# Performance work log

Measured on AMD Instinct MI355X. Metric: run time of the kernel, lower is better.

Reference implementation:

```python
import jax, jax.numpy as jnp
import numpy as np

BS, N, C = 512, 18, 2048
EPS = 1e-12
BN_SCALE = 1.0 / np.sqrt(1.0 + 1e-5)  # eval-mode BN with running_mean=0, running_var=1


def _normalize(v):
    # F.normalize(p=2, dim=2, eps=1e-12)
    n = jnp.linalg.norm(v, axis=2, keepdims=True)
    return v / jnp.maximum(n, EPS)


def _bn_relu(v, gamma, beta):
    # BatchNorm2d in eval mode (running_mean=0, running_var=1) followed by ReLU
    return jax.nn.relu(v * (gamma * BN_SCALE) + beta)


def _safe_sqrt(r):
    # forward-identical to sqrt (r >= 0 here); avoids NaN grad at r == 0 (diagonal)
    pos = r > 0
    return jnp.where(pos, jnp.sqrt(jnp.where(pos, r, 1.0)), 0.0)


def setup_inputs() -> dict:
    key = jax.random.key(0)
    ks = jax.random.split(key, 10)
    s = 0.02
    return {
        "x": jax.random.normal(ks[0], (BS, N, C), jnp.float32),
        "part_coordinate": jax.random.uniform(ks[1], (BS, N, 4), jnp.float32),
        # conv1: C -> 3 (1x1)
        "w1": jax.random.normal(ks[2], (3, C), jnp.float32) * s,
        "b1": jnp.zeros((3,), jnp.float32),
        # conv2: 4 -> C, BN, ReLU, C -> 3
        "w2a": jax.random.normal(ks[3], (C, 4), jnp.float32) * s,
        "b2a": jnp.zeros((C,), jnp.float32),
        "g2": jnp.ones((C,), jnp.float32),
        "be2": jnp.zeros((C,), jnp.float32),
        "w2b": jax.random.normal(ks[4], (3, C), jnp.float32) * s,
        "b2b": jnp.zeros((3,), jnp.float32),
        # conv: C -> C, BN, ReLU
        "wc": jax.random.normal(ks[5], (C, C), jnp.float32) * s,
        "bc": jnp.zeros((C,), jnp.float32),
        "gc": jnp.ones((C,), jnp.float32),
        "bec": jnp.zeros((C,), jnp.float32),
        # conv3: C -> C, BN, ReLU
        "w3": jax.random.normal(ks[6], (C, C), jnp.float32) * s,
        "b3": jnp.zeros((C,), jnp.float32),
        "g3": jnp.ones((C,), jnp.float32),
        "be3": jnp.zeros((C,), jnp.float32),
    }


def reference(x, part_coordinate, w1, b1, w2a, b2a, g2, be2, w2b, b2b,
              wc, bc, gc, bec, w3, b3, g3, be3):
    # z1 = softmax(conv1(x)) over the 3 clusters
    z1 = jax.nn.softmax(jnp.einsum('bnc,kc->bnk', x, w1) + b1, axis=2)  # [B,N,3]

    # distance_list1: cosine affinities of x and z1
    xn = _normalize(x)
    d1_1 = jnp.einsum('bnc,bmc->bnm', xn, xn)       # [B,N,N]
    z1n = _normalize(z1)
    d2_1 = jnp.einsum('bnk,bmk->bnm', z1n, z1n)     # [B,N,N]

    # z2 = softmax(conv2(part_coordinate))
    h = _bn_relu(jnp.einsum('bnf,cf->bnc', part_coordinate, w2a) + b2a, g2, be2)
    z2 = jax.nn.softmax(jnp.einsum('bnc,kc->bnk', h, w2b) + b2b, axis=2)  # [B,N,3]

    # distance_list2: spatial-center distance + cosine affinity of z2
    yc = part_coordinate[..., 0] + jnp.floor(part_coordinate[..., 2] / 2)
    xc = part_coordinate[..., 1] + jnp.floor(part_coordinate[..., 3] / 2)
    dy = (yc[:, None, :] - yc[:, :, None]) ** 2
    dx = (xc[:, None, :] - xc[:, :, None]) ** 2
    d1_2 = 1.0 - 2.0 * _safe_sqrt(dx + dy)          # [B,N,N]
    z2n = _normalize(z2)
    d2_2 = jnp.einsum('bnk,bmk->bnm', z2n, z2n)     # [B,N,N]

    # encode / decode aggregation over 3 cluster nodes
    z = z1 + z2                                      # [B,N,3]
    enc = z / (jnp.sum(z, axis=1, keepdims=True) + EPS)
    dec = z / (jnp.sum(z, axis=2, keepdims=True) + EPS)
    u = jnp.einsum('bnk,bnc->bkc', enc, x)           # [B,3,C]
    u = _bn_relu(jnp.einsum('bkc,dc->bkd', u, wc) + bc, gc, bec)
    y = jnp.einsum('bnk,bkc->bnc', dec, u)           # [B,N,C]
    y = _bn_relu(jnp.einsum('bnc,dc->bnd', y, w3) + b3, g3, be3) + x

    return (y, d2_1, d1_1, d2_2, d1_2)
```

## Files before the change

kernel.cpp:

```cpp
#include <hip/hip_runtime.h>

#define BS   512
#define NPTS 18
#define CH   2048
#define EPSF 1e-12f
#define BNS  0.9999950000374997f

typedef unsigned short ushort_t;
typedef __attribute__((ext_vector_type(8)))  short bfrag;
typedef __attribute__((ext_vector_type(4)))  float f32x4v;
typedef __attribute__((ext_vector_type(16))) float f32x16;

__device__ inline ushort_t bf16_rne(float f) {
  union { float f; unsigned int u; } c; c.f = f;
  unsigned int u = c.u;
  u += 0x7fffu + ((u >> 16) & 1u);
  return (ushort_t)(u >> 16);
}
__device__ inline float bf16_to_f(ushort_t s) {
  union { float f; unsigned int u; } c; c.u = ((unsigned int)s) << 16;
  return c.f;
}
__device__ inline bfrag cvt8(float4 a, float4 b) {
  bfrag r;
  r[0]=(short)bf16_rne(a.x); r[1]=(short)bf16_rne(a.y);
  r[2]=(short)bf16_rne(a.z); r[3]=(short)bf16_rne(a.w);
  r[4]=(short)bf16_rne(b.x); r[5]=(short)bf16_rne(b.y);
  r[6]=(short)bf16_rne(b.z); r[7]=(short)bf16_rne(b.w);
  return r;
}

__global__ __launch_bounds__(256) void k_fused(
    const float* __restrict__ x, const float* __restrict__ pc,
    const float* __restrict__ w1,
    const float* __restrict__ w2a, const float* __restrict__ b2a,
    const float* __restrict__ g2, const float* __restrict__ be2,
    const float* __restrict__ w2b,
    const float* __restrict__ wc, const float* __restrict__ w3,
    ushort_t* __restrict__ wc_bf, ushort_t* __restrict__ w3_bf,
    float* __restrict__ Glp, float* __restrict__ l2p)
{
  const int blk = blockIdx.x, tid = threadIdx.x;

  if (blk >= BS*4) {
    const int cb = blk - BS*4;
    const int n4 = CH*CH/4;
    #pragma unroll
    for (int k = 0; k < 4; k++) {
      int gid = (cb*4 + k)*256 + tid;
      const float* src; ushort_t* dst; int i;
      if (gid < n4) { src = wc; dst = wc_bf; i = gid; }
      else          { src = w3; dst = w3_bf; i = gid - n4; }
      float4 v = ((const float4*)src)[i];
      ushort4 o;
      o.x = bf16_rne(v.x); o.y = bf16_rne(v.y);
      o.z = bf16_rne(v.z); o.w = bf16_rne(v.w);
      ((ushort4*)dst)[i] = o;
    }
    return;
  }

  __shared__ float Gt[4][378];
  const int bq = blk, b = bq >> 2, q = bq & 3;
  const int lane = tid & 63, wv = tid >> 6;

  {
    const int rc = lane & 31, kh = lane >> 5;
    const int arow = (rc < NPTS) ? rc : (NPTS-1);
    const bool isw = (rc >= NPTS) && (rc < NPTS+3);
    const int wrow = isw ? (rc - NPTS) : 0;
    const float* xp = x + ((size_t)b*NPTS + arow)*CH + q*512 + wv*128 + kh*8;
    const float* wp = w1 + (size_t)wrow*CH + q*512 + wv*128 + kh*8;
    f32x16 acc0 = {0.f,0.f,0.f,0.f,0.f,0.f,0.f,0.f,0.f,0.f,0.f,0.f,0.f,0.f,0.f,0.f};
    f32x16 acc1 = acc0;
    #pragma unroll
    for (int j = 0; j < 8; j++) {
      const int kb = j*16;
      bfrag av = cvt8(*(const float4*)(xp + kb), *(const float4*)(xp + kb + 4));
      bfrag bv = av;
      if (isw) bv = cvt8(*(const float4*)(wp + kb), *(const float4*)(wp + kb + 4));
      if (j & 1) acc1 = __builtin_amdgcn_mfma_f32_32x32x16_bf16(av, bv, acc1, 0, 0, 0);
      else       acc0 = __builtin_amdgcn_mfma_f32_32x32x16_bf16(av, bv, acc0, 0, 0, 0);
    }
    #pragma unroll
    for (int r = 0; r < 16; r++) {
      int orow = (r & 3) + 8*(r >> 2) + 4*kh;
      if (orow < NPTS && rc < 21) Gt[wv][orow*21 + rc] = acc0[r] + acc1[r];
    }
  }

  {
    const int p0 = wv*5;
    const int np = (wv == 3) ? 3 : 5;
    float4 pq[5];
    #pragma unroll
    for (int j = 0; j < 5; j++)
      pq[j] = *(const float4*)(pc + (size_t)b*NPTS*4 + (p0 + (j < np ? j : 0))*4);
    float acc[5][3];
    #pragma unroll
    for (int j = 0; j < 5; j++) { acc[j][0]=0.f; acc[j][1]=0.f; acc[j][2]=0.f; }
    #pragma unroll 2
    for (int it = 0; it < 8; it++) {
      int c = q*512 + it*64 + lane;
      const float4 wa = *(const float4*)(w2a + (size_t)c*4);
      float bb = b2a[c], gg = g2[c]*BNS, be = be2[c];
      float wb0 = w2b[c], wb1 = w2b[CH+c], wb2 = w2b[2*CH+c];
      #pragma unroll
      for (int j = 0; j < 5; j++) {
        float v = fmaf(pq[j].w, wa.w, fmaf(pq[j].z, wa.z,
                  fmaf(pq[j].y, wa.y, fmaf(pq[j].x, wa.x, bb))));
        float h = fmaxf(fmaf(v, gg, be), 0.f);
        acc[j][0] = fmaf(h, wb0, acc[j][0]);
        acc[j][1] = fmaf(h, wb1, acc[j][1]);
        acc[j][2] = fmaf(h, wb2, acc[j][2]);
      }
    }
    #pragma unroll
    for (int j = 0; j < 5; j++) {
      if (j < np) {
        #pragma unroll
        for (int k = 0; k < 3; k++) {
          float v = acc[j][k];
          #pragma unroll
          for (int off = 32; off; off >>= 1) v += __shfl_xor(v, off);
          if (lane == 0) l2p[(size_t)bq*54 + (p0+j)*3 + k] = v;
        }
      }
    }
  }

  __syncthreads();
  for (int t = tid; t < 378; t += 256) {
    float* g = Glp + (size_t)bq*378;
    g[t] = (Gt[0][t] + Gt[1][t]) + (Gt[2][t] + Gt[3][t]);
  }
}

__global__ __launch_bounds__(512) void k_final(
    const float* __restrict__ x, const float* __restrict__ pc,
    const float* __restrict__ b1, const float* __restrict__ b2b,
    const float* __restrict__ Glp, const float* __restrict__ l2p,
    float* __restrict__ d21, float* __restrict__ d11,
    float* __restrict__ d22, float* __restrict__ d12,
    ushort_t* __restrict__ u_pre, float* __restrict__ dec_out)
{
  __shared__ float sGl[378];
  __shared__ float l2s[54];
  __shared__ float z1s[54], z2s[54], encs[54];
  __shared__ float ycs[NPTS], xcs[NPTS];
  __shared__ float n1inv[NPTS], n2inv[NPTS], rinv[NPTS], colinv[3];
  const int b = blockIdx.x, tid = threadIdx.x;

  if (tid < 378) {
    const float* g = Glp + (size_t)b*4*378 + tid;
    sGl[tid] = (g[0] + g[378]) + (g[756] + g[1134]);
  } else if (tid < 432) {
    int t = tid - 378;
    const float* g = l2p + (size_t)b*4*54 + t;
    l2s[t] = (g[0] + g[54]) + (g[108] + g[162]) + b2b[t%3];
  } else if (tid < 450) {
    int n = tid - 432;
    const float* p = pc + (size_t)b*NPTS*4 + n*4;
    ycs[n] = p[0] + floorf(p[2]*0.5f);
    xcs[n] = p[1] + floorf(p[3]*0.5f);
  }
  __syncthreads();

  if (tid < NPTS) {
    int n = tid;
    float a0 = sGl[n*21+18] + b1[0], a1 = sGl[n*21+19] + b1[1], a2 = sGl[n*21+20] + b1[2];
    float mx = fmaxf(a0, fmaxf(a1, a2));
    float e0 = expf(a0-mx), e1 = expf(a1-mx), e2 = expf(a2-mx);
    float inv = 1.f/(e0+e1+e2);
    float z10 = e0*inv, z11 = e1*inv, z12 = e2*inv;
    z1s[n*3+0]=z10; z1s[n*3+1]=z11; z1s[n*3+2]=z12;
    n1inv[n] = 1.f/fmaxf(sqrtf(z10*z10+z11*z11+z12*z12), EPSF);

    float c0 = l2s[n*3+0], c1 = l2s[n*3+1], c2 = l2s[n*3+2];
    mx = fmaxf(c0, fmaxf(c1, c2));
    e0 = expf(c0-mx); e1 = expf(c1-mx); e2 = expf(c2-mx);
    inv = 1.f/(e0+e1+e2);
    float z20 = e0*inv, z21 = e1*inv, z22 = e2*inv;
    z2s[n*3+0]=z20; z2s[n*3+1]=z21; z2s[n*3+2]=z22;
    n2inv[n] = 1.f/fmaxf(sqrtf(z20*z20+z21*z21+z22*z22), EPSF);

    float zr0 = z10+z20, zr1 = z11+z21, zr2 = z12+z22;
    float rinvv = 1.f/((zr0+zr1+zr2) + EPSF);
    dec_out[(size_t)b*54 + n*3 + 0] = zr0*rinvv;
    dec_out[(size_t)b*54 + n*3 + 1] = zr1*rinvv;
    dec_out[(size_t)b*54 + n*3 + 2] = zr2*rinvv;

    rinv[n] = 1.f/fmaxf(sqrtf(sGl[n*21+n]), EPSF);
  }
  __syncthreads();

  if (tid < 3) {
    float s = 0.f;
    #pragma unroll
    for (int n = 0; n < NPTS; n++) s += z1s[n*3+tid] + z2s[n*3+tid];
    colinv[tid] = 1.f/(s + EPSF);
  }
  if (tid < NPTS*NPTS) {
    int t = tid;
    int n = t/NPTS, mm = t - n*NPTS;
    float dd21 = (z1s[n*3]*z1s[mm*3] + z1s[n*3+1]*z1s[mm*3+1] + z1s[n*3+2]*z1s[mm*3+2])
                 * n1inv[n]*n1inv[mm];
    float dd22 = (z2s[n*3]*z2s[mm*3] + z2s[n*3+1]*z2s[mm*3+1] + z2s[n*3+2]*z2s[mm*3+2])
                 * n2inv[n]*n2inv[mm];
    float dd11 = sGl[n*21+mm] * rinv[n]*rinv[mm];
    float dyv = ycs[mm]-ycs[n], dxv = xcs[mm]-xcs[n];
    float r = dxv*dxv + dyv*dyv;
    float dd12 = 1.f - 2.f*((r > 0.f) ? sqrtf(r) : 0.f);
    size_t o = (size_t)b*NPTS*NPTS + t;
    d21[o] = dd21; d11[o] = dd11; d22[o] = dd22; d12[o] = dd12;
  }
  __syncthreads();
  if (tid < 54) encs[tid] = (z1s[tid]+z2s[tid])*colinv[tid%3];
  __syncthreads();

  {
    const int c0 = tid*4;
    const float* xb = x + (size_t)b*NPTS*CH + c0;
    float av0[4], av1[4], av2[4];
    #pragma unroll
    for (int j = 0; j < 4; j++) { av0[j]=0.f; av1[j]=0.f; av2[j]=0.f; }
    #pragma unroll 2
    for (int n = 0; n < NPTS; n++) {
      float4 xv = *(const float4*)(xb + (size_t)n*CH);
      float e0 = encs[n*3+0], e1 = encs[n*3+1], e2 = encs[n*3+2];
      av0[0]=fmaf(e0,xv.x,av0[0]); av0[1]=fmaf(e0,xv.y,av0[1]);
      av0[2]=fmaf(e0,xv.z,av0[2]); av0[3]=fmaf(e0,xv.w,av0[3]);
      av1[0]=fmaf(e1,xv.x,av1[0]); av1[1]=fmaf(e1,xv.y,av1[1]);
      av1[2]=fmaf(e1,xv.z,av1[2]); av1[3]=fmaf(e1,xv.w,av1[3]);
      av2[0]=fmaf(e2,xv.x,av2[0]); av2[1]=fmaf(e2,xv.y,av2[1]);
      av2[2]=fmaf(e2,xv.z,av2[2]); av2[3]=fmaf(e2,xv.w,av2[3]);
    }
    ushort4 o0, o1, o2;
    o0.x=bf16_rne(av0[0]); o0.y=bf16_rne(av0[1]); o0.z=bf16_rne(av0[2]); o0.w=bf16_rne(av0[3]);
    o1.x=bf16_rne(av1[0]); o1.y=bf16_rne(av1[1]); o1.z=bf16_rne(av1[2]); o1.w=bf16_rne(av1[3]);
    o2.x=bf16_rne(av2[0]); o2.y=bf16_rne(av2[1]); o2.z=bf16_rne(av2[2]); o2.w=bf16_rne(av2[3]);
    *(ushort4*)(u_pre + ((size_t)b*3 + 0)*CH + c0) = o0;
    *(ushort4*)(u_pre + ((size_t)b*3 + 1)*CH + c0) = o1;
    *(ushort4*)(u_pre + ((size_t)b*3 + 2)*CH + c0) = o2;
  }
}

#define GM 1536
#define GK 2048
#define GN 2048

#define STAGE(buf, k0) { \
    _Pragma("unroll") \
    for (int i = 0; i < 4; i++) \
      __builtin_amdgcn_global_load_lds( \
          (const __attribute__((address_space(1))) void*)(Ag + (size_t)(i*32 + ldrow)*GK + (k0)), \
          (__attribute__((address_space(3))) void*)(&Asm[buf][i*2048 + wv*512]), 16, 0, 0); \
    _Pragma("unroll") \
    for (int i = 0; i < 2; i++) \
      __builtin_amdgcn_global_load_lds( \
          (const __attribute__((address_space(1))) void*)(Bg + (size_t)(i*32 + ldrow)*GK + (k0)), \
          (__attribute__((address_space(3))) void*)(&Bsm[buf][i*2048 + wv*512]), 16, 0, 0); }

template<int MODE>
__global__ __launch_bounds__(256) void gemm_mfma(
    const ushort_t* __restrict__ A, const ushort_t* __restrict__ B,
    void* __restrict__ Cout, const float* __restrict__ bias,
    const float* __restrict__ gamma, const float* __restrict__ beta)
{
  __shared__ ushort_t Asm[2][128*64];
  __shared__ ushort_t Bsm[2][64*64];
  const int tid  = threadIdx.x;
  const int lane = tid & 63, wv = tid >> 6;
  const int mb = blockIdx.x % (GM/128), nb = blockIdx.x / (GM/128);
  const int wr = (wv >> 1) * 64, wc = (wv & 1) * 32;

  f32x4v acc[4][2];
  #pragma unroll
  for (int m = 0; m < 4; m++)
    #pragma unroll
    for (int n = 0; n < 2; n++)
      acc[m][n] = (f32x4v){0.f, 0.f, 0.f, 0.f};

  const int ldrow = tid >> 3;
  const int ldcol = (((tid & 7) ^ (ldrow & 7)) * 8);
  const ushort_t* Ag = A + (size_t)(mb*128)*GK + ldcol;
  const ushort_t* Bg = B + (size_t)(nb*64)*GK + ldcol;
  const int r15 = lane & 15, khi = lane >> 4;

  STAGE(0, 0)
  __syncthreads();
  for (int t = 0; t < GK/64; ++t) {
    const int cur = t & 1;
    if (t < GK/64 - 1) STAGE(cur ^ 1, (t+1)*64)
    #pragma unroll
    for (int ks = 0; ks < 2; ks++) {
      bfrag af[4], bfv[2];
      #pragma unroll
      for (int m = 0; m < 4; m++) {
        const int ar = wr + m*16 + r15;
        af[m] = *(const bfrag*)(&Asm[cur][ar*64 + ((ks*32 + khi*8) ^ ((ar & 7)*8))]);
      }
      #pragma unroll
      for (int n = 0; n < 2; n++) {
        const int br = wc + n*16 + r15;
        bfv[n] = *(const bfrag*)(&Bsm[cur][br*64 + ((ks*32 + khi*8) ^ ((br & 7)*8))]);
      }
      #pragma unroll
      for (int m = 0; m < 4; m++)
        #pragma unroll
        for (int n = 0; n < 2; n++)
          acc[m][n] = __builtin_amdgcn_mfma_f32_16x16x32_bf16(
              af[m], bfv[n], acc[m][n], 0, 0, 0);
    }
    __syncthreads();
  }

  #pragma unroll
  for (int n = 0; n < 2; n++) {
    const int gc = nb*64 + wc + n*16 + r15;
    float bi = 0.f, ga = 0.f, be = 0.f;
    if (MODE == 1) { bi = bias[gc]; ga = gamma[gc]*BNS; be = beta[gc]; }
    #pragma unroll
    for (int m = 0; m < 4; m++) {
      const int gr0 = mb*128 + wr + m*16 + khi*4;
      #pragma unroll
      for (int r = 0; r < 4; r++) {
        float v = acc[m][n][r];
        if (MODE == 1) {
          v = fmaxf(fmaf(v + bi, ga, be), 0.f);
          ((ushort_t*)Cout)[(size_t)(gr0 + r)*GN + gc] = bf16_rne(v);
        } else {
          ((float*)Cout)[(size_t)(gr0 + r)*GN + gc] = v;
        }
      }
    }
  }
}

__global__ __launch_bounds__(256) void k_epi(
    const float* __restrict__ x, const float* __restrict__ V,
    const float* __restrict__ dec, const float* __restrict__ b3,
    const float* __restrict__ g3, const float* __restrict__ be3,
    float* __restrict__ y)
{
  __shared__ float4 lv[3*512];
  __shared__ float4 lmul[512], ladd[512];
  __shared__ float ld[54];
  const int b = blockIdx.x, tid = threadIdx.x;

  const float4* v4 = (const float4*)(V + (size_t)b*3*CH);
  for (int i = tid; i < 1536; i += 256) lv[i] = v4[i];
  const float4* g34  = (const float4*)g3;
  const float4* b34  = (const float4*)b3;
  const float4* be34 = (const float4*)be3;
  for (int i = tid; i < 512; i += 256) {
    float4 g = g34[i], bb = b34[i], be = be34[i];
    float4 mu, ad;
    mu.x = g.x*BNS; mu.y = g.y*BNS; mu.z = g.z*BNS; mu.w = g.w*BNS;
    ad.x = fmaf(bb.x, mu.x, be.x); ad.y = fmaf(bb.y, mu.y, be.y);
    ad.z = fmaf(bb.z, mu.z, be.z); ad.w = fmaf(bb.w, mu.w, be.w);
    lmul[i] = mu; ladd[i] = ad;
  }
  if (tid < 54) ld[tid] = dec[(size_t)b*54 + tid];
  __syncthreads();

  for (int r = 0; r < NPTS; r++) {
    float d0 = ld[r*3+0], d1 = ld[r*3+1], d2 = ld[r*3+2];
    const float4* xr = (const float4*)(x + ((size_t)b*NPTS + r)*CH);
    float4* yr = (float4*)(y + ((size_t)b*NPTS + r)*CH);
    for (int i = tid; i < 512; i += 256) {
      float4 v0 = lv[i], v1 = lv[512+i], v2 = lv[1024+i];
      float4 mu = lmul[i], ad = ladd[i], xa = xr[i];
      float4 o;
      o.x = fmaxf(fmaf(fmaf(d0,v0.x, fmaf(d1,v1.x, d2*v2.x)), mu.x, ad.x), 0.f) + xa.x;
      o.y = fmaxf(fmaf(fmaf(d0,v0.y, fmaf(d1,v1.y, d2*v2.y)), mu.y, ad.y), 0.f) + xa.y;
      o.z = fmaxf(fmaf(fmaf(d0,v0.z, fmaf(d1,v1.z, d2*v2.z)), mu.z, ad.z), 0.f) + xa.z;
      o.w = fmaxf(fmaf(fmaf(d0,v0.w, fmaf(d1,v1.w, d2*v2.w)), mu.w, ad.w), 0.f) + xa.w;
      yr[i] = o;
    }
  }
}

extern "C" void kernel_launch(void* const* d_in, const int* in_sizes, int n_in,
                              void* d_out, int out_size, void* d_ws, size_t ws_size,
                              hipStream_t stream) {
  const float* x   = (const float*)d_in[0];
  const float* pc  = (const float*)d_in[1];
  const float* w1  = (const float*)d_in[2];
  const float* b1  = (const float*)d_in[3];
  const float* w2a = (const float*)d_in[4];
  const float* b2a = (const float*)d_in[5];
  const float* g2  = (const float*)d_in[6];
  const float* be2 = (const float*)d_in[7];
  const float* w2b = (const float*)d_in[8];
  const float* b2b = (const float*)d_in[9];
  const float* wc  = (const float*)d_in[10];
  const float* bc  = (const float*)d_in[11];
  const float* gc  = (const float*)d_in[12];
  const float* bec = (const float*)d_in[13];
  const float* w3  = (const float*)d_in[14];
  const float* b3  = (const float*)d_in[15];
  const float* g3  = (const float*)d_in[16];
  const float* be3 = (const float*)d_in[17];

  float* out = (float*)d_out;
  float* y   = out;
  float* d21 = out + (size_t)BS*NPTS*CH;
  float* d11 = d21 + (size_t)BS*NPTS*NPTS;
  float* d22 = d11 + (size_t)BS*NPTS*NPTS;
  float* d12 = d22 + (size_t)BS*NPTS*NPTS;

  char* ybytes = (char*)y;
  ushort_t* u_pre_bf = (ushort_t*)(ybytes + 0);
  ushort_t* u_bf     = (ushort_t*)(ybytes + 6291456);
  ushort_t* wc_bf    = (ushort_t*)(ybytes + 12582912);
  ushort_t* w3_bf    = (ushort_t*)(ybytes + 20971520);
  float*    Glp      = (float*)   (ybytes + 29360128);
  float*    l2p      = (float*)   (ybytes + 32456704);

  float* V    = (float*)d_ws;
  float* decb = V + (size_t)BS*3*CH;

  k_fused<<<BS*4 + 2048, 256, 0, stream>>>(x, pc, w1, w2a, b2a, g2, be2, w2b,
                                           wc, w3, wc_bf, w3_bf, Glp, l2p);
  k_final<<<BS, 512, 0, stream>>>(x, pc, b1, b2b, Glp, l2p,
                                  d21, d11, d22, d12, u_pre_bf, decb);
  gemm_mfma<1><<<(GM/128)*(GN/64), 256, 0, stream>>>(u_pre_bf, wc_bf, u_bf, bc, gc, bec);
  gemm_mfma<0><<<(GM/128)*(GN/64), 256, 0, stream>>>(u_bf, w3_bf, V, nullptr, nullptr, nullptr);
  k_epi<<<BS, 256, 0, stream>>>(x, V, decb, b3, g3, be3, y);
}
```

Before: 158.9 us.

## Fuse Gram and finalize kernels into one per-batch kernel with LDS-staged bf16 x

Merges the partial-Gram/coordinate-MLP kernel and the finalize kernel into a single 1024-thread block per batch. The block converts x and w1 to bf16 into a swizzled LDS image, then runs the Gram MFMAs and the encoder reduction from that image. This removes the global round-trip of partial sums and the second read of x. In exchange it uses about 86KB of LDS per block, which limits occupancy and leaves many waves idle during the MFMA phase. It also accumulates u_pre from bf16-rounded x, which lowers precision.

```diff
diff --git a/kernel.cpp b/kernel.cpp
--- a/kernel.cpp
+++ b/kernel.cpp
@@ -30,24 +30,26 @@
   return r;
 }
 
-__global__ __launch_bounds__(256) void k_fused(
+__global__ __launch_bounds__(1024, 4) void k_mega(
     const float* __restrict__ x, const float* __restrict__ pc,
-    const float* __restrict__ w1,
+    const float* __restrict__ w1, const float* __restrict__ b1,
     const float* __restrict__ w2a, const float* __restrict__ b2a,
     const float* __restrict__ g2, const float* __restrict__ be2,
-    const float* __restrict__ w2b,
+    const float* __restrict__ w2b, const float* __restrict__ b2b,
     const float* __restrict__ wc, const float* __restrict__ w3,
     ushort_t* __restrict__ wc_bf, ushort_t* __restrict__ w3_bf,
-    float* __restrict__ Glp, float* __restrict__ l2p)
+    float* __restrict__ d21, float* __restrict__ d11,
+    float* __restrict__ d22, float* __restrict__ d12,
+    ushort_t* __restrict__ u_pre, float* __restrict__ dec_out)
 {
   const int blk = blockIdx.x, tid = threadIdx.x;
 
-  if (blk >= BS*4) {
-    const int cb = blk - BS*4;
+  if (blk >= BS) {
+    const int cb = blk - BS;
     const int n4 = CH*CH/4;
     #pragma unroll
     for (int k = 0; k < 4; k++) {
-      int gid = (cb*4 + k)*256 + tid;
+      int gid = cb*4096 + k*1024 + tid;
       const float* src; ushort_t* dst; int i;
       if (gid < n4) { src = wc; dst = wc_bf; i = gid; }
       else          { src = w3; dst = w3_bf; i = gid - n4; }
@@ -60,25 +62,54 @@
     return;
   }
 
+  __shared__ __align__(16) ushort_t IMG[21*CH];
   __shared__ float Gt[4][378];
-  const int bq = blk, b = bq >> 2, q = bq & 3;
-  const int lane = tid & 63, wv = tid >> 6;
+  __shared__ float l2part[9][18];
+  __shared__ float sGl[378], l2s[54];
+  __shared__ float z1s[54], z2s[54], encs[54];
+  __shared__ float ycs[NPTS], xcs[NPTS];
+  __shared__ float n1inv[NPTS], n2inv[NPTS], rinvS[NPTS], colinv[3];
+
+  const int b = blk, lane = tid & 63, wv = tid >> 6;
 
   {
+    const float4* x4 = (const float4*)x + (size_t)b*9216;
+    #pragma unroll
+    for (int k = 0; k < 4; k++) {
+      int p = k*1024 + tid;
+      float4 a = x4[2*p], c = x4[2*p + 1];
+      int row = p >> 8;
+      *(bfrag*)((char*)IMG + ((p*16) ^ ((row & 7) << 4))) = cvt8(a, c);
+    }
+    if (tid < 512) {
+      int p = 4096 + tid;
+      float4 a = x4[2*p], c = x4[2*p + 1];
+      int row = p >> 8;
+      *(bfrag*)((char*)IMG + ((p*16) ^ ((row & 7) << 4))) = cvt8(a, c);
+    }
+    if (tid < 768) {
+      int p = tid;
+      const float4* w4 = (const float4*)w1;
+      float4 a = w4[2*p], c = w4[2*p + 1];
+      int row = 18 + (p >> 8);
+      *(bfrag*)((char*)IMG + ((73728 + p*16) ^ ((row & 7) << 4))) = cvt8(a, c);
+    }
+  }
+  __syncthreads();
+
+  if (wv < 4) {
     const int rc = lane & 31, kh = lane >> 5;
     const int arow = (rc < NPTS) ? rc : (NPTS-1);
-    const bool isw = (rc >= NPTS) && (rc < NPTS+3);
-    const int wrow = isw ? (rc - NPTS) : 0;
-    const float* xp = x + ((size_t)b*NPTS + arow)*CH + q*512 + wv*128 + kh*8;
-    const float* wp = w1 + (size_t)wrow*CH + q*512 + wv*128 + kh*8;
+    const int brow = (rc < 21) ? rc : 20;
+    const int amsk = (arow & 7) << 4, bmsk = (brow & 7) << 4;
+    const int abase = arow*4096, bbase = brow*4096;
     f32x16 acc0 = {0.f,0.f,0.f,0.f,0.f,0.f,0.f,0.f,0.f,0.f,0.f,0.f,0.f,0.f,0.f,0.f};
     f32x16 acc1 = acc0;
-    #pragma unroll
-    for (int j = 0; j < 8; j++) {
-      const int kb = j*16;
-      bfrag av = cvt8(*(const float4*)(xp + kb), *(const float4*)(xp + kb + 4));
-      bfrag bv = av;
-      if (isw) bv = cvt8(*(const float4*)(wp + kb), *(const float4*)(wp + kb + 4));
+    #pragma unroll 4
+    for (int j = 0; j < 32; j++) {
+      const int kb = (wv*512 + j*16 + kh*8)*2;
+      bfrag av = *(const bfrag*)((const char*)IMG + ((abase + kb) ^ amsk));
+      bfrag bv = *(const bfrag*)((const char*)IMG + ((bbase + kb) ^ bmsk));
       if (j & 1) acc1 = __builtin_amdgcn_mfma_f32_32x32x16_bf16(av, bv, acc1, 0, 0, 0);
       else       acc0 = __builtin_amdgcn_mfma_f32_32x32x16_bf16(av, bv, acc0, 0, 0, 0);
     }
@@ -87,28 +118,28 @@
       int orow = (r & 3) + 8*(r >> 2) + 4*kh;
       if (orow < NPTS && rc < 21) Gt[wv][orow*21 + rc] = acc0[r] + acc1[r];
     }
-  }
-
-  {
-    const int p0 = wv*5;
-    const int np = (wv == 3) ? 3 : 5;
-    float4 pq[5];
-    #pragma unroll
-    for (int j = 0; j < 5; j++)
-      pq[j] = *(const float4*)(pc + (size_t)b*NPTS*4 + (p0 + (j < np ? j : 0))*4);
-    float acc[5][3];
-    #pragma unroll
-    for (int j = 0; j < 5; j++) { acc[j][0]=0.f; acc[j][1]=0.f; acc[j][2]=0.f; }
-    #pragma unroll 2
-    for (int it = 0; it < 8; it++) {
-      int c = q*512 + it*64 + lane;
+  } else if (wv < 13) {
+    const int zid = wv - 4, g = zid/3, th = zid - 3*g;
+    const int cs = (th == 0) ? 0 : (th == 1) ? 683 : 1366;
+    const int ce = (th == 0) ? 683 : (th == 1) ? 1366 : 2048;
+    const float* pcb = pc + (size_t)b*NPTS*4 + g*24;
+    float pq[6][4];
+    #pragma unroll
+    for (int j = 0; j < 6; j++) {
+      pq[j][0] = pcb[j*4+0]; pq[j][1] = pcb[j*4+1];
+      pq[j][2] = pcb[j*4+2]; pq[j][3] = pcb[j*4+3];
+    }
+    float acc[6][3];
+    #pragma unroll
+    for (int j = 0; j < 6; j++) { acc[j][0]=0.f; acc[j][1]=0.f; acc[j][2]=0.f; }
+    for (int c = cs + lane; c < ce; c += 64) {
       const float4 wa = *(const float4*)(w2a + (size_t)c*4);
       float bb = b2a[c], gg = g2[c]*BNS, be = be2[c];
       float wb0 = w2b[c], wb1 = w2b[CH+c], wb2 = w2b[2*CH+c];
       #pragma unroll
-      for (int j = 0; j < 5; j++) {
-        float v = fmaf(pq[j].w, wa.w, fmaf(pq[j].z, wa.z,
-                  fmaf(pq[j].y, wa.y, fmaf(pq[j].x, wa.x, bb))));
+      for (int j = 0; j < 6; j++) {
+        float v = fmaf(pq[j][3], wa.w, fmaf(pq[j][2], wa.z,
+                  fmaf(pq[j][1], wa.y, fmaf(pq[j][0], wa.x, bb))));
         float h = fmaxf(fmaf(v, gg, be), 0.f);
         acc[j][0] = fmaf(h, wb0, acc[j][0]);
         acc[j][1] = fmaf(h, wb1, acc[j][1]);
@@ -116,50 +147,26 @@
       }
     }
     #pragma unroll
-    for (int j = 0; j < 5; j++) {
-      if (j < np) {
+    for (int j = 0; j < 6; j++)
+      #pragma unroll
+      for (int k = 0; k < 3; k++) {
+        float v = acc[j][k];
         #pragma unroll
-        for (int k = 0; k < 3; k++) {
-          float v = acc[j][k];
-          #pragma unroll
-          for (int off = 32; off; off >>= 1) v += __shfl_xor(v, off);
-          if (lane == 0) l2p[(size_t)bq*54 + (p0+j)*3 + k] = v;
-        }
+        for (int off = 32; off; off >>= 1) v += __shfl_xor(v, off);
+        if (lane == 0) l2part[zid][j*3 + k] = v;
       }
-    }
-  }
-
-  __syncthreads();
-  for (int t = tid; t < 378; t += 256) {
-    float* g = Glp + (size_t)bq*378;
-    g[t] = (Gt[0][t] + Gt[1][t]) + (Gt[2][t] + Gt[3][t]);
-  }
-}
-
-__global__ __launch_bounds__(512) void k_final(
-    const float* __restrict__ x, const float* __restrict__ pc,
-    const float* __restrict__ b1, const float* __restrict__ b2b,
-    const float* __restrict__ Glp, const float* __restrict__ l2p,
-    float* __restrict__ d21, float* __restrict__ d11,
-    float* __restrict__ d22, float* __restrict__ d12,
-    ushort_t* __restrict__ u_pre, float* __restrict__ dec_out)
-{
-  __shared__ float sGl[378];
-  __shared__ float l2s[54];
-  __shared__ float z1s[54], z2s[54], encs[54];
-  __shared__ float ycs[NPTS], xcs[NPTS];
-  __shared__ float n1inv[NPTS], n2inv[NPTS], rinv[NPTS], colinv[3];
-  const int b = blockIdx.x, tid = threadIdx.x;
+  }
+  __syncthreads();
 
   if (tid < 378) {
-    const float* g = Glp + (size_t)b*4*378 + tid;
-    sGl[tid] = (g[0] + g[378]) + (g[756] + g[1134]);
+    sGl[tid] = (Gt[0][tid] + Gt[1][tid]) + (Gt[2][tid] + Gt[3][tid]);
   } else if (tid < 432) {
     int t = tid - 378;
-    const float* g = l2p + (size_t)b*4*54 + t;
-    l2s[t] = (g[0] + g[54]) + (g[108] + g[162]) + b2b[t%3];
-  } else if (tid < 450) {
-    int n = tid - 432;
+    int p = t/3, k = t - 3*p, g = p/6, pp = p - 6*g;
+    l2s[t] = l2part[g*3][pp*3+k] + l2part[g*3+1][pp*3+k] + l2part[g*3+2][pp*3+k]
+             + b2b[k];
+  } else if (tid >= 448 && tid < 466) {
+    int n = tid - 448;
     const float* p = pc + (size_t)b*NPTS*4 + n*4;
     ycs[n] = p[0] + floorf(p[2]*0.5f);
     xcs[n] = p[1] + floorf(p[3]*0.5f);
@@ -190,7 +197,7 @@
     dec_out[(size_t)b*54 + n*3 + 1] = zr1*rinvv;
     dec_out[(size_t)b*54 + n*3 + 2] = zr2*rinvv;
 
-    rinv[n] = 1.f/fmaxf(sqrtf(sGl[n*21+n]), EPSF);
+    rinvS[n] = 1.f/fmaxf(sqrtf(sGl[n*21+n]), EPSF);
   }
   __syncthreads();
 
@@ -207,7 +214,7 @@
                  * n1inv[n]*n1inv[mm];
     float dd22 = (z2s[n*3]*z2s[mm*3] + z2s[n*3+1]*z2s[mm*3+1] + z2s[n*3+2]*z2s[mm*3+2])
                  * n2inv[n]*n2inv[mm];
-    float dd11 = sGl[n*21+mm] * rinv[n]*rinv[mm];
+    float dd11 = sGl[n*21+mm] * rinvS[n]*rinvS[mm];
     float dyv = ycs[mm]-ycs[n], dxv = xcs[mm]-xcs[n];
     float r = dxv*dxv + dyv*dyv;
     float dd12 = 1.f - 2.f*((r > 0.f) ? sqrtf(r) : 0.f);
@@ -219,29 +226,25 @@
   __syncthreads();
 
   {
-    const int c0 = tid*4;
-    const float* xb = x + (size_t)b*NPTS*CH + c0;
-    float av0[4], av1[4], av2[4];
-    #pragma unroll
-    for (int j = 0; j < 4; j++) { av0[j]=0.f; av1[j]=0.f; av2[j]=0.f; }
-    #pragma unroll 2
+    const int c0 = tid*2;
+    float a0=0.f,a1=0.f,a2=0.f, q0=0.f,q1=0.f,q2=0.f;
+    #pragma unroll
     for (int n = 0; n < NPTS; n++) {
-      float4 xv = *(const float4*)(xb + (size_t)n*CH);
+      unsigned v = *(const unsigned*)((const char*)IMG + ((n*4096 + c0*2) ^ ((n & 7) << 4)));
+      float x0 = bf16_to_f((ushort_t)(v & 0xffff));
+      float x1 = bf16_to_f((ushort_t)(v >> 16));
       float e0 = encs[n*3+0], e1 = encs[n*3+1], e2 = encs[n*3+2];
-      av0[0]=fmaf(e0,xv.x,av0[0]); av0[1]=fmaf(e0,xv.y,av0[1]);
-      av0[2]=fmaf(e0,xv.z,av0[2]); av0[3]=fmaf(e0,xv.w,av0[3]);
-      av1[0]=fmaf(e1,xv.x,av1[0]); av1[1]=fmaf(e1,xv.y,av1[1]);
-      av1[2]=fmaf(e1,xv.z,av1[2]); av1[3]=fmaf(e1,xv.w,av1[3]);
-      av2[0]=fmaf(e2,xv.x,av2[0]); av2[1]=fmaf(e2,xv.y,av2[1]);
-      av2[2]=fmaf(e2,xv.z,av2[2]); av2[3]=fmaf(e2,xv.w,av2[3]);
-    }
-    ushort4 o0, o1, o2;
-    o0.x=bf16_rne(av0[0]); o0.y=bf16_rne(av0[1]); o0.z=bf16_rne(av0[2]); o0.w=bf16_rne(av0[3]);
-    o1.x=bf16_rne(av1[0]); o1.y=bf16_rne(av1[1]); o1.z=bf16_rne(av1[2]); o1.w=bf16_rne(av1[3]);
-    o2.x=bf16_rne(av2[0]); o2.y=bf16_rne(av2[1]); o2.z=bf16_rne(av2[2]); o2.w=bf16_rne(av2[3]);
-    *(ushort4*)(u_pre + ((size_t)b*3 + 0)*CH + c0) = o0;
-    *(ushort4*)(u_pre + ((size_t)b*3 + 1)*CH + c0) = o1;
-    *(ushort4*)(u_pre + ((size_t)b*3 + 2)*CH + c0) = o2;
+      a0 = fmaf(e0, x0, a0); q0 = fmaf(e0, x1, q0);
+      a1 = fmaf(e1, x0, a1); q1 = fmaf(e1, x1, q1);
+      a2 = fmaf(e2, x0, a2); q2 = fmaf(e2, x1, q2);
+    }
+    ushort2 o0, o1, o2;
+    o0.x = bf16_rne(a0); o0.y = bf16_rne(q0);
+    o1.x = bf16_rne(a1); o1.y = bf16_rne(q1);
+    o2.x = bf16_rne(a2); o2.y = bf16_rne(q2);
+    *(ushort2*)(u_pre + ((size_t)b*3 + 0)*CH + c0) = o0;
+    *(ushort2*)(u_pre + ((size_t)b*3 + 1)*CH + c0) = o1;
+    *(ushort2*)(u_pre + ((size_t)b*3 + 2)*CH + c0) = o2;
   }
 }
 
@@ -415,16 +418,13 @@
   ushort_t* u_bf     = (ushort_t*)(ybytes + 6291456);
   ushort_t* wc_bf    = (ushort_t*)(ybytes + 12582912);
   ushort_t* w3_bf    = (ushort_t*)(ybytes + 20971520);
-  float*    Glp      = (float*)   (ybytes + 29360128);
-  float*    l2p      = (float*)   (ybytes + 32456704);
 
   float* V    = (float*)d_ws;
   float* decb = V + (size_t)BS*3*CH;
 
-  k_fused<<<BS*4 + 2048, 256, 0, stream>>>(x, pc, w1, w2a, b2a, g2, be2, w2b,
-                                           wc, w3, wc_bf, w3_bf, Glp, l2p);
-  k_final<<<BS, 512, 0, stream>>>(x, pc, b1, b2b, Glp, l2p,
-                                  d21, d11, d22, d12, u_pre_bf, decb);
+  k_mega<<<BS + 512, 1024, 0, stream>>>(x, pc, w1, b1, w2a, b2a, g2, be2,
+                                        w2b, b2b, wc, w3, wc_bf, w3_bf,
+                                        d21, d11, d22, d12, u_pre_bf, decb);
   gemm_mfma<1><<<(GM/128)*(GN/64), 256, 0, stream>>>(u_pre_bf, wc_bf, u_bf, bc, gc, bec);
   gemm_mfma<0><<<(GM/128)*(GN/64), 256, 0, stream>>>(u_bf, w3_bf, V, nullptr, nullptr, nullptr);
   k_epi<<<BS, 256, 0, stream>>>(x, V, decb, b3, g3, be3, y);
```

Measured after the change: 150.8 us. 5.1% less time.
